# Optimization experiments

Measured on AMD Instinct MI355X. Metric: run time of the kernel, lower is better.

The kernel has to match this reference:

```python
import jax, jax.numpy as jnp
import numpy as np

N = 50000   # nodes
E = 800000  # edges (avg degree 16)
F_IN = 128
D_HID = 128
N_CLASS = 40


def setup_inputs() -> dict:
    key = jax.random.key(0)
    ks = jax.random.split(key, 10)
    s = 0.05
    return {
        "x": jax.random.normal(ks[0], (N, F_IN), jnp.float32),
        "edge_index": jax.random.randint(ks[1], (2, E), 0, N, dtype=jnp.int32),
        "W_in": jax.random.normal(ks[2], (F_IN, D_HID), jnp.float32) * s,
        "b_in": jnp.zeros((D_HID,), jnp.float32),
        "W1": jax.random.normal(ks[3], (D_HID, D_HID), jnp.float32) * s,
        "b1": jnp.zeros((D_HID,), jnp.float32),
        "W2": jax.random.normal(ks[4], (D_HID, D_HID), jnp.float32) * s,
        "b2": jnp.zeros((D_HID,), jnp.float32),
        "W_out": jax.random.normal(ks[5], (D_HID, N_CLASS), jnp.float32) * s,
        "b_out": jnp.zeros((N_CLASS,), jnp.float32),
    }


def _gcn_norm(edge_index, num_nodes):
    # Add self loops, compute symmetric normalization D^-1/2 (A+I) D^-1/2.
    loop = jnp.arange(num_nodes, dtype=edge_index.dtype)
    src = jnp.concatenate([edge_index[0], loop])
    dst = jnp.concatenate([edge_index[1], loop])
    deg = jnp.zeros((num_nodes,), jnp.float32).at[dst].add(1.0)
    dinv = jnp.where(deg > 0, jax.lax.rsqrt(deg), 0.0)
    norm = dinv[src] * dinv[dst]  # [E+N]
    return src, dst, norm


def _gcn_conv(h, W, b, src, dst, norm, num_nodes):
    # transform then sparse aggregate (gather-scale-scatter)
    h = h @ W                                   # [N, d]
    msg = h[src] * norm[:, None]                # [E+N, d]
    agg = jax.ops.segment_sum(msg, dst, num_segments=num_nodes)
    return agg + b


def reference(x, edge_index, W_in, b_in, W1, b1, W2, b2, W_out, b_out):
    num_nodes = x.shape[0]
    src, dst, norm = _gcn_norm(edge_index, num_nodes)
    h = _gcn_conv(x, W_in, b_in, src, dst, norm, num_nodes)
    # eval mode: dropout is identity
    h = jax.nn.relu(_gcn_conv(h, W1, b1, src, dst, norm, num_nodes))
    h = jax.nn.relu(_gcn_conv(h, W2, b2, src, dst, norm, num_nodes))
    out = h @ W_out + b_out
    return jax.nn.log_softmax(out, axis=1)
```

## Files before the change

### kernel.cpp

```cpp
#include <hip/hip_runtime.h>
#include <hip/hip_bf16.h>
#include <math.h>

#define NEG_INF (-3.402823466e38f)
typedef unsigned int uint;
typedef unsigned short ushort;
typedef __attribute__((ext_vector_type(8))) short short8;
typedef __attribute__((ext_vector_type(4))) float f32x4;

__device__ __forceinline__ float bf_lo(uint u) { return __uint_as_float(u << 16); }
__device__ __forceinline__ float bf_hi(uint u) { return __uint_as_float(u & 0xffff0000u); }
__device__ __forceinline__ ushort f2bf(float f) {
  __hip_bfloat16 h = __float2bfloat16(f);
  return *reinterpret_cast<ushort*>(&h);
}
__device__ __forceinline__ uint pack2(float a, float b) {
  return (uint)f2bf(a) | ((uint)f2bf(b) << 16);
}

__global__ __launch_bounds__(256) void k_pcnt(
    const float* __restrict__ W_in, const float* __restrict__ W1,
    const float* __restrict__ W2, ushort* __restrict__ Wt,
    const int* __restrict__ edges, int* __restrict__ cnt8, int E, int n)
{
  int b = blockIdx.x;
  if (b < 24) {
    const float* W = (b < 8) ? W_in : (b < 16) ? W1 : W2;
    ushort* dst = Wt + (size_t)(b >> 3) * 16384;
    int id = (b & 7) * 256 + threadIdx.x;
    int col = id >> 4, kc = id & 15;
    const float* src = W + (size_t)(kc * 8) * 128 + col;
    uint4 pk;
    pk.x = pack2(src[0],       src[128]);
    pk.y = pack2(src[2 * 128], src[3 * 128]);
    pk.z = pack2(src[4 * 128], src[5 * 128]);
    pk.w = pack2(src[6 * 128], src[7 * 128]);
    ((uint4*)dst)[id] = pk;
  } else {
    int cb = b - 24;
    int* my = cnt8 + (size_t)(cb & 7) * n;
    int stride = ((int)gridDim.x - 24) * 256;
    for (int e = cb * 256 + threadIdx.x; e < E; e += stride)
      atomicAdd(&my[edges[E + e]], 1);
  }
}

__global__ void k_dinv(const int* __restrict__ cnt8, int* __restrict__ cnt,
                       float* __restrict__ dinv, int n) {
  int i = blockIdx.x * 256 + threadIdx.x;
  if (i < n) {
    int s = 0;
    #pragma unroll
    for (int p = 0; p < 8; ++p) s += cnt8[(size_t)p * n + i];
    cnt[i] = s;
    dinv[i] = rsqrtf((float)s + 1.0f);
  }
}

__global__ __launch_bounds__(256) void k_gf(
    const float* __restrict__ A, const ushort* __restrict__ Wt,
    const float* __restrict__ dinv, ushort* __restrict__ T, int n, int gb,
    const int* __restrict__ edges, int* __restrict__ cfill,
    int* __restrict__ csr, int E, int npp, int nbp)
{
  __shared__ ushort sW[128 * 128];
  int tid = threadIdx.x;

  if ((int)blockIdx.x >= gb) {
    int b2 = blockIdx.x - gb;
    int part = b2 & 7;
    int lo = part * npp, hi = lo + npp;
    int stride = nbp * 256;
    int e = (b2 >> 3) * 256 + tid;
    for (; e + 3 * stride < E; e += 4 * stride) {
      int d0 = edges[E + e];
      int d1 = edges[E + e + stride];
      int d2 = edges[E + e + 2 * stride];
      int d3 = edges[E + e + 3 * stride];
      if (d0 >= lo && d0 < hi) { int s = edges[e];              int p0 = atomicAdd(&cfill[d0], 1); if (p0 < 64) csr[((size_t)d0 << 6) + p0] = s; }
      if (d1 >= lo && d1 < hi) { int s = edges[e + stride];     int p1 = atomicAdd(&cfill[d1], 1); if (p1 < 64) csr[((size_t)d1 << 6) + p1] = s; }
      if (d2 >= lo && d2 < hi) { int s = edges[e + 2 * stride]; int p2 = atomicAdd(&cfill[d2], 1); if (p2 < 64) csr[((size_t)d2 << 6) + p2] = s; }
      if (d3 >= lo && d3 < hi) { int s = edges[e + 3 * stride]; int p3 = atomicAdd(&cfill[d3], 1); if (p3 < 64) csr[((size_t)d3 << 6) + p3] = s; }
    }
    for (; e < E; e += stride) {
      int d = edges[E + e];
      if (d >= lo && d < hi) { int s = edges[e]; int p0 = atomicAdd(&cfill[d], 1); if (p0 < 64) csr[((size_t)d << 6) + p0] = s; }
    }
    return;
  }

  {
    const uint4* Wt4 = (const uint4*)Wt;
    uint4* sW4 = (uint4*)sW;
    #pragma unroll
    for (int j = 0; j < 8; ++j) {
      int id = j * 256 + tid;
      int col = id >> 4, kc = id & 15;
      sW4[(col << 4) | (kc ^ (col & 7))] = Wt4[id];
    }
  }
  __syncthreads();

  int wid = tid >> 6, lane = tid & 63;
  int lr = lane & 15, lg = lane >> 4;
  int rbase = blockIdx.x * 64 + wid * 16;
  int arow = rbase + lr;
  bool valid = arow < n;

  f32x4 acc[8];
  #pragma unroll
  for (int cf = 0; cf < 8; ++cf) acc[cf] = (f32x4){0.f, 0.f, 0.f, 0.f};

  #pragma unroll
  for (int ks = 0; ks < 4; ++ks) {
    short8 a = {};
    if (valid) {
      const float4* Af = (const float4*)(A + (size_t)arow * 128) + (ks * 4 + lg) * 2;
      float4 u = Af[0], w = Af[1];
      union { uint4 u4; short8 s8; } cv;
      cv.u4.x = pack2(u.x, u.y); cv.u4.y = pack2(u.z, u.w);
      cv.u4.z = pack2(w.x, w.y); cv.u4.w = pack2(w.z, w.w);
      a = cv.s8;
    }
    int kc = (ks << 2) | lg;
    #pragma unroll
    for (int cf = 0; cf < 8; ++cf) {
      int col = (cf << 4) | lr;
      const short8* bp = (const short8*)sW + ((col << 4) | (kc ^ (lr & 7)));
      acc[cf] = __builtin_amdgcn_mfma_f32_16x16x32_bf16(a, *bp, acc[cf], 0, 0, 0);
    }
  }

  #pragma unroll
  for (int v = 0; v < 4; ++v) {
    int row = rbase + (lg << 2) + v;
    if (row < n) {
      float s = dinv[row];
      ushort* dst = T + (size_t)row * 128 + lr;
      #pragma unroll
      for (int cf = 0; cf < 8; ++cf) dst[cf << 4] = f2bf(acc[cf][v] * s);
    }
  }
}

__global__ __launch_bounds__(256) void k_gemm(
    const ushort* __restrict__ Ap, const ushort* __restrict__ Wt,
    const float* __restrict__ dinv, ushort* __restrict__ T, int n)
{
  __shared__ ushort sW[128 * 128];
  int tid = threadIdx.x;
  {
    const uint4* Wt4 = (const uint4*)Wt;
    uint4* sW4 = (uint4*)sW;
    #pragma unroll
    for (int j = 0; j < 8; ++j) {
      int id = j * 256 + tid;
      int col = id >> 4, kc = id & 15;
      sW4[(col << 4) | (kc ^ (col & 7))] = Wt4[id];
    }
  }
  __syncthreads();

  int wid = tid >> 6, lane = tid & 63;
  int lr = lane & 15, lg = lane >> 4;
  int rbase = blockIdx.x * 64 + wid * 16;
  int arow = rbase + lr;
  bool valid = arow < n;

  f32x4 acc[8];
  #pragma unroll
  for (int cf = 0; cf < 8; ++cf) acc[cf] = (f32x4){0.f, 0.f, 0.f, 0.f};

  #pragma unroll
  for (int ks = 0; ks < 4; ++ks) {
    short8 a = {};
    if (valid) a = ((const short8*)(Ap + (size_t)arow * 128))[ks * 4 + lg];
    int kc = (ks << 2) | lg;
    #pragma unroll
    for (int cf = 0; cf < 8; ++cf) {
      int col = (cf << 4) | lr;
      const short8* bp = (const short8*)sW + ((col << 4) | (kc ^ (lr & 7)));
      acc[cf] = __builtin_amdgcn_mfma_f32_16x16x32_bf16(a, *bp, acc[cf], 0, 0, 0);
    }
  }

  #pragma unroll
  for (int v = 0; v < 4; ++v) {
    int row = rbase + (lg << 2) + v;
    if (row < n) {
      float s = dinv[row];
      ushort* dst = T + (size_t)row * 128 + lr;
      #pragma unroll
      for (int cf = 0; cf < 8; ++cf) dst[cf << 4] = f2bf(acc[cf][v] * s);
    }
  }
}

template <int RELU>
__global__ __launch_bounds__(256) void k_agg(
    const ushort* __restrict__ T, const int* __restrict__ cnt,
    const int* __restrict__ csr, const float* __restrict__ dinv,
    const float* __restrict__ bias, ushort* __restrict__ H, int n)
{
  int u = (blockIdx.x << 2) + (threadIdx.x >> 6);
  if (u >= n) return;
  int lane = threadIdx.x & 63;
  const uint* Tu = (const uint*)T;
  uint su = Tu[(size_t)u * 64 + lane];
  float ax = bf_lo(su), ay = bf_hi(su);
  int deg = cnt[u];
  int dcap = deg > 64 ? 64 : deg;
  int eid = (lane < dcap) ? csr[((size_t)u << 6) + lane] : 0;
  int j = 0;
  for (; j + 16 <= dcap; j += 16) {
    uint v[16];
    #pragma unroll
    for (int q = 0; q < 16; ++q) {
      int s = __shfl(eid, j + q);
      v[q] = Tu[(size_t)s * 64 + lane];
    }
    float sx = 0.f, sy = 0.f;
    #pragma unroll
    for (int q = 0; q < 16; ++q) { sx += bf_lo(v[q]); sy += bf_hi(v[q]); }
    ax += sx; ay += sy;
  }
  for (; j + 4 <= dcap; j += 4) {
    int s0 = __shfl(eid, j);     int s1 = __shfl(eid, j + 1);
    int s2 = __shfl(eid, j + 2); int s3 = __shfl(eid, j + 3);
    uint v0 = Tu[(size_t)s0 * 64 + lane];
    uint v1 = Tu[(size_t)s1 * 64 + lane];
    uint v2 = Tu[(size_t)s2 * 64 + lane];
    uint v3 = Tu[(size_t)s3 * 64 + lane];
    ax += (bf_lo(v0) + bf_lo(v1)) + (bf_lo(v2) + bf_lo(v3));
    ay += (bf_hi(v0) + bf_hi(v1)) + (bf_hi(v2) + bf_hi(v3));
  }
  for (; j < dcap; ++j) {
    int s = __shfl(eid, j);
    uint v = Tu[(size_t)s * 64 + lane];
    ax += bf_lo(v); ay += bf_hi(v);
  }
  float du = dinv[u];
  float2 b2 = *(const float2*)(bias + (lane << 1));
  float ox = fmaf(ax, du, b2.x);
  float oy = fmaf(ay, du, b2.y);
  if (RELU) { ox = fmaxf(ox, 0.f); oy = fmaxf(oy, 0.f); }
  ((uint*)H)[(size_t)u * 64 + lane] = pack2(ox, oy);
}

__global__ __launch_bounds__(256) void k_head(
    const ushort* __restrict__ H, const float* __restrict__ Wo,
    const float* __restrict__ bo, float* __restrict__ out, int n)
{
  __shared__ float sWo[128 * 40];
  __shared__ float sX[128 * 64];
  int tid = threadIdx.x;
  int rbase = blockIdx.x * 64;

  {
    const float4* Wo4 = (const float4*)Wo;
    float4* sWo4 = (float4*)sWo;
    #pragma unroll
    for (int i = 0; i < 5; ++i) sWo4[i * 256 + tid] = Wo4[i * 256 + tid];
  }
  {
    const uint4* H4 = (const uint4*)H;
    #pragma unroll
    for (int j = 0; j < 4; ++j) {
      int id = j * 256 + tid;
      int r = id & 63, kc8 = id >> 6;
      int row = rbase + r;
      uint4 v = make_uint4(0u, 0u, 0u, 0u);
      if (row < n) v = H4[(size_t)row * 16 + kc8];
      float f[8] = {bf_lo(v.x), bf_hi(v.x), bf_lo(v.y), bf_hi(v.y),
                    bf_lo(v.z), bf_hi(v.z), bf_lo(v.w), bf_hi(v.w)};
      #pragma unroll
      for (int j2 = 0; j2 < 8; ++j2) {
        int k = kc8 * 8 + j2;
        int swz = ((k >> 2) & 7) << 2;
        sX[k * 64 + (r ^ swz)] = f[j2];
      }
    }
  }
  __syncthreads();

  int cg = tid & 7;
  int rg = tid >> 3;
  float bj[5];
  #pragma unroll
  for (int j = 0; j < 5; ++j) bj[j] = bo[cg * 5 + j];
  float acc[2][5];
  #pragma unroll
  for (int i = 0; i < 2; ++i)
    #pragma unroll
    for (int j = 0; j < 5; ++j) acc[i][j] = bj[j];

  #pragma unroll 4
  for (int k = 0; k < 128; ++k) {
    int swz = ((k >> 2) & 7) << 2;
    float2 xv = *(const float2*)(sX + k * 64 + ((rg << 1) ^ swz));
    const float* wr = sWo + k * 40 + cg * 5;
    float w0 = wr[0], w1 = wr[1], w2 = wr[2], w3 = wr[3], w4 = wr[4];
    acc[0][0] = fmaf(xv.x, w0, acc[0][0]);
    acc[0][1] = fmaf(xv.x, w1, acc[0][1]);
    acc[0][2] = fmaf(xv.x, w2, acc[0][2]);
    acc[0][3] = fmaf(xv.x, w3, acc[0][3]);
    acc[0][4] = fmaf(xv.x, w4, acc[0][4]);
    acc[1][0] = fmaf(xv.y, w0, acc[1][0]);
    acc[1][1] = fmaf(xv.y, w1, acc[1][1]);
    acc[1][2] = fmaf(xv.y, w2, acc[1][2]);
    acc[1][3] = fmaf(xv.y, w3, acc[1][3]);
    acc[1][4] = fmaf(xv.y, w4, acc[1][4]);
  }

  #pragma unroll
  for (int i = 0; i < 2; ++i) {
    int row = rbase + (rg << 1) + i;
    float m = acc[i][0];
    m = fmaxf(m, acc[i][1]); m = fmaxf(m, acc[i][2]);
    m = fmaxf(m, acc[i][3]); m = fmaxf(m, acc[i][4]);
    m = fmaxf(m, __shfl_xor(m, 1));
    m = fmaxf(m, __shfl_xor(m, 2));
    m = fmaxf(m, __shfl_xor(m, 4));
    float s = 0.f;
    #pragma unroll
    for (int j = 0; j < 5; ++j) s += __expf(acc[i][j] - m);
    s += __shfl_xor(s, 1);
    s += __shfl_xor(s, 2);
    s += __shfl_xor(s, 4);
    float ls = m + __logf(s);
    if (row < n) {
      float* dst = out + (size_t)row * 40 + cg * 5;
      #pragma unroll
      for (int j = 0; j < 5; ++j) dst[j] = acc[i][j] - ls;
    }
  }
}

extern "C" void kernel_launch(void* const* d_in, const int* in_sizes, int n_in,
                              void* d_out, int out_size, void* d_ws, size_t ws_size,
                              hipStream_t stream) {
  const float* x    = (const float*)d_in[0];
  const int*   edges= (const int*)d_in[1];
  const float* W_in = (const float*)d_in[2];
  const float* b_in = (const float*)d_in[3];
  const float* W1   = (const float*)d_in[4];
  const float* b1   = (const float*)d_in[5];
  const float* W2   = (const float*)d_in[6];
  const float* b2   = (const float*)d_in[7];
  const float* Wo   = (const float*)d_in[8];
  const float* bo   = (const float*)d_in[9];
  float* out = (float*)d_out;

  int N = in_sizes[0] / 128;
  int E = in_sizes[1] / 2;
  int NB = (N + 255) / 256;

  char* p = (char*)d_ws;
  auto alloc = [&](size_t bytes) {
    char* r = p; p += (bytes + 255) & ~(size_t)255; return r;
  };
  ushort* t    = (ushort*)alloc((size_t)N * 128 * 2);
  ushort* h    = (ushort*)alloc((size_t)N * 128 * 2);
  ushort* wt   = (ushort*)alloc(3 * 16384 * 2);
  int*   cnt8  = (int*)  alloc((size_t)N * 9 * 4);
  int*   cfill = cnt8 + (size_t)N * 8;
  int*   cnt   = (int*)  alloc((size_t)N * 4);
  float* dinv  = (float*)alloc((size_t)N * 4);
  int*   csr   = (int*)  alloc((size_t)N * 64 * 4);
  (void)ws_size; (void)n_in; (void)out_size;

  int NPP = (N + 7) / 8;
  int NBP = 512;
  int GB  = (N + 63) / 64;
  int AB  = (N + 3) / 4;

  hipMemsetAsync(cnt8, 0, (size_t)N * 9 * 4, stream);
  k_pcnt<<<24 + 2048, 256, 0, stream>>>(W_in, W1, W2, wt, edges, cnt8, E, N);
  k_dinv<<<NB, 256, 0, stream>>>(cnt8, cnt, dinv, N);
  k_gf  <<<GB + NBP * 8, 256, 0, stream>>>(x, wt, dinv, t, N, GB,
                                           edges, cfill, csr, E, NPP, NBP);
  k_agg<0><<<AB, 256, 0, stream>>>(t, cnt, csr, dinv, b_in, h, N);
  k_gemm<<<GB, 256, 0, stream>>>(h, wt + 16384, dinv, t, N);
  k_agg<1><<<AB, 256, 0, stream>>>(t, cnt, csr, dinv, b1, h, N);
  k_gemm<<<GB, 256, 0, stream>>>(h, wt + 2 * 16384, dinv, t, N);
  k_agg<1><<<AB, 256, 0, stream>>>(t, cnt, csr, dinv, b2, h, N);
  k_head<<<GB, 256, 0, stream>>>(h, Wo, bo, out, N);
}
```

Baseline: 224.2 us.

## Drop separate degree-count pass; apply source normalization inside aggregation

Removes the separate edge-degree counting kernel and takes degrees from the CSR fill counters, so dinv is computed after the fused GEMM/CSR-build kernel. Because dinv is no longer known when the GEMM runs, source-side scaling moves out of the GEMM epilogues into the aggregation loop. There each neighbor's dinv is gathered once per lane and broadcast by shuffle, and self-loop scaling is handled separately. Weight conversion to bf16 is folded into the fused kernel. This saves one full pass over the edge list of atomics and a memset of eight count copies. In exchange it adds a dinv gather and extra shuffles per edge in every aggregation.

```diff
diff --git a/kernel.cpp b/kernel.cpp
--- a/kernel.cpp
+++ b/kernel.cpp
@@ -18,56 +18,24 @@
   return (uint)f2bf(a) | ((uint)f2bf(b) << 16);
 }
 
-__global__ __launch_bounds__(256) void k_pcnt(
-    const float* __restrict__ W_in, const float* __restrict__ W1,
-    const float* __restrict__ W2, ushort* __restrict__ Wt,
-    const int* __restrict__ edges, int* __restrict__ cnt8, int E, int n)
-{
-  int b = blockIdx.x;
-  if (b < 24) {
-    const float* W = (b < 8) ? W_in : (b < 16) ? W1 : W2;
-    ushort* dst = Wt + (size_t)(b >> 3) * 16384;
-    int id = (b & 7) * 256 + threadIdx.x;
-    int col = id >> 4, kc = id & 15;
-    const float* src = W + (size_t)(kc * 8) * 128 + col;
-    uint4 pk;
-    pk.x = pack2(src[0],       src[128]);
-    pk.y = pack2(src[2 * 128], src[3 * 128]);
-    pk.z = pack2(src[4 * 128], src[5 * 128]);
-    pk.w = pack2(src[6 * 128], src[7 * 128]);
-    ((uint4*)dst)[id] = pk;
-  } else {
-    int cb = b - 24;
-    int* my = cnt8 + (size_t)(cb & 7) * n;
-    int stride = ((int)gridDim.x - 24) * 256;
-    for (int e = cb * 256 + threadIdx.x; e < E; e += stride)
-      atomicAdd(&my[edges[E + e]], 1);
-  }
-}
-
-__global__ void k_dinv(const int* __restrict__ cnt8, int* __restrict__ cnt,
-                       float* __restrict__ dinv, int n) {
+__global__ void k_dinv(const int* __restrict__ cfill, float* __restrict__ dinv, int n) {
   int i = blockIdx.x * 256 + threadIdx.x;
-  if (i < n) {
-    int s = 0;
-    #pragma unroll
-    for (int p = 0; p < 8; ++p) s += cnt8[(size_t)p * n + i];
-    cnt[i] = s;
-    dinv[i] = rsqrtf((float)s + 1.0f);
-  }
+  if (i < n) dinv[i] = rsqrtf((float)cfill[i] + 1.0f);
 }
 
 __global__ __launch_bounds__(256) void k_gf(
-    const float* __restrict__ A, const ushort* __restrict__ Wt,
-    const float* __restrict__ dinv, ushort* __restrict__ T, int n, int gb,
+    const float* __restrict__ A, const float* __restrict__ W_in,
+    const float* __restrict__ W1, const float* __restrict__ W2,
+    ushort* __restrict__ Wt, ushort* __restrict__ T, int n, int gb,
     const int* __restrict__ edges, int* __restrict__ cfill,
     int* __restrict__ csr, int E, int npp, int nbp)
 {
   __shared__ ushort sW[128 * 128];
   int tid = threadIdx.x;
-
-  if ((int)blockIdx.x >= gb) {
-    int b2 = blockIdx.x - gb;
+  int bid = blockIdx.x;
+
+  if (bid >= gb + 16) {
+    int b2 = bid - gb - 16;
     int part = b2 & 7;
     int lo = part * npp, hi = lo + npp;
     int stride = nbp * 256;
@@ -89,21 +57,42 @@
     return;
   }
 
+  if (bid >= gb) {
+    int b2 = bid - gb;
+    const float* W = (b2 < 8) ? W1 : W2;
+    ushort* dst = Wt + (size_t)(b2 >> 3) * 16384;
+    int id = (b2 & 7) * 256 + tid;
+    int col = id >> 4, kc = id & 15;
+    const float* src = W + (size_t)(kc * 8) * 128 + col;
+    uint4 pk;
+    pk.x = pack2(src[0],       src[128]);
+    pk.y = pack2(src[2 * 128], src[3 * 128]);
+    pk.z = pack2(src[4 * 128], src[5 * 128]);
+    pk.w = pack2(src[6 * 128], src[7 * 128]);
+    ((uint4*)dst)[id] = pk;
+    return;
+  }
+
   {
-    const uint4* Wt4 = (const uint4*)Wt;
     uint4* sW4 = (uint4*)sW;
     #pragma unroll
     for (int j = 0; j < 8; ++j) {
       int id = j * 256 + tid;
       int col = id >> 4, kc = id & 15;
-      sW4[(col << 4) | (kc ^ (col & 7))] = Wt4[id];
+      const float* src = W_in + (size_t)(kc * 8) * 128 + col;
+      uint4 pk;
+      pk.x = pack2(src[0],       src[128]);
+      pk.y = pack2(src[2 * 128], src[3 * 128]);
+      pk.z = pack2(src[4 * 128], src[5 * 128]);
+      pk.w = pack2(src[6 * 128], src[7 * 128]);
+      sW4[(col << 4) | (kc ^ (col & 7))] = pk;
     }
   }
   __syncthreads();
 
   int wid = tid >> 6, lane = tid & 63;
   int lr = lane & 15, lg = lane >> 4;
-  int rbase = blockIdx.x * 64 + wid * 16;
+  int rbase = bid * 64 + wid * 16;
   int arow = rbase + lr;
   bool valid = arow < n;
 
@@ -135,17 +124,16 @@
   for (int v = 0; v < 4; ++v) {
     int row = rbase + (lg << 2) + v;
     if (row < n) {
-      float s = dinv[row];
       ushort* dst = T + (size_t)row * 128 + lr;
       #pragma unroll
-      for (int cf = 0; cf < 8; ++cf) dst[cf << 4] = f2bf(acc[cf][v] * s);
+      for (int cf = 0; cf < 8; ++cf) dst[cf << 4] = f2bf(acc[cf][v]);
     }
   }
 }
 
 __global__ __launch_bounds__(256) void k_gemm(
     const ushort* __restrict__ Ap, const ushort* __restrict__ Wt,
-    const float* __restrict__ dinv, ushort* __restrict__ T, int n)
+    ushort* __restrict__ T, int n)
 {
   __shared__ ushort sW[128 * 128];
   int tid = threadIdx.x;
@@ -188,17 +176,16 @@
   for (int v = 0; v < 4; ++v) {
     int row = rbase + (lg << 2) + v;
     if (row < n) {
-      float s = dinv[row];
       ushort* dst = T + (size_t)row * 128 + lr;
       #pragma unroll
-      for (int cf = 0; cf < 8; ++cf) dst[cf << 4] = f2bf(acc[cf][v] * s);
+      for (int cf = 0; cf < 8; ++cf) dst[cf << 4] = f2bf(acc[cf][v]);
     }
   }
 }
 
 template <int RELU>
 __global__ __launch_bounds__(256) void k_agg(
-    const ushort* __restrict__ T, const int* __restrict__ cnt,
+    const ushort* __restrict__ T, const int* __restrict__ cfill,
     const int* __restrict__ csr, const float* __restrict__ dinv,
     const float* __restrict__ bias, ushort* __restrict__ H, int n)
 {
@@ -207,42 +194,53 @@
   int lane = threadIdx.x & 63;
   const uint* Tu = (const uint*)T;
   uint su = Tu[(size_t)u * 64 + lane];
-  float ax = bf_lo(su), ay = bf_hi(su);
-  int deg = cnt[u];
+  int deg = cfill[u];
   int dcap = deg > 64 ? 64 : deg;
-  int eid = (lane < dcap) ? csr[((size_t)u << 6) + lane] : 0;
+  int eid = 0; float ds = 0.f;
+  if (lane < dcap) {
+    eid = csr[((size_t)u << 6) + lane];
+    ds  = dinv[eid];
+  }
+  float ax = 0.f, ay = 0.f;
   int j = 0;
   for (; j + 16 <= dcap; j += 16) {
-    uint v[16];
+    uint v[16]; float w[16];
     #pragma unroll
     for (int q = 0; q < 16; ++q) {
       int s = __shfl(eid, j + q);
+      w[q] = __shfl(ds, j + q);
       v[q] = Tu[(size_t)s * 64 + lane];
     }
-    float sx = 0.f, sy = 0.f;
-    #pragma unroll
-    for (int q = 0; q < 16; ++q) { sx += bf_lo(v[q]); sy += bf_hi(v[q]); }
-    ax += sx; ay += sy;
+    #pragma unroll
+    for (int q = 0; q < 16; ++q) {
+      ax = fmaf(w[q], bf_lo(v[q]), ax);
+      ay = fmaf(w[q], bf_hi(v[q]), ay);
+    }
   }
   for (; j + 4 <= dcap; j += 4) {
-    int s0 = __shfl(eid, j);     int s1 = __shfl(eid, j + 1);
-    int s2 = __shfl(eid, j + 2); int s3 = __shfl(eid, j + 3);
+    int s0 = __shfl(eid, j);     float w0 = __shfl(ds, j);
+    int s1 = __shfl(eid, j + 1); float w1 = __shfl(ds, j + 1);
+    int s2 = __shfl(eid, j + 2); float w2 = __shfl(ds, j + 2);
+    int s3 = __shfl(eid, j + 3); float w3 = __shfl(ds, j + 3);
     uint v0 = Tu[(size_t)s0 * 64 + lane];
     uint v1 = Tu[(size_t)s1 * 64 + lane];
     uint v2 = Tu[(size_t)s2 * 64 + lane];
     uint v3 = Tu[(size_t)s3 * 64 + lane];
-    ax += (bf_lo(v0) + bf_lo(v1)) + (bf_lo(v2) + bf_lo(v3));
-    ay += (bf_hi(v0) + bf_hi(v1)) + (bf_hi(v2) + bf_hi(v3));
+    ax = fmaf(w0, bf_lo(v0), fmaf(w1, bf_lo(v1), fmaf(w2, bf_lo(v2), fmaf(w3, bf_lo(v3), ax))));
+    ay = fmaf(w0, bf_hi(v0), fmaf(w1, bf_hi(v1), fmaf(w2, bf_hi(v2), fmaf(w3, bf_hi(v3), ay))));
   }
   for (; j < dcap; ++j) {
     int s = __shfl(eid, j);
+    float w = __shfl(ds, j);
     uint v = Tu[(size_t)s * 64 + lane];
-    ax += bf_lo(v); ay += bf_hi(v);
+    ax = fmaf(w, bf_lo(v), ax);
+    ay = fmaf(w, bf_hi(v), ay);
   }
   float du = dinv[u];
+  float sw = du * du;
   float2 b2 = *(const float2*)(bias + (lane << 1));
-  float ox = fmaf(ax, du, b2.x);
-  float oy = fmaf(ay, du, b2.y);
+  float ox = fmaf(du, ax, fmaf(sw, bf_lo(su), b2.x));
+  float oy = fmaf(du, ay, fmaf(sw, bf_hi(su), b2.y));
   if (RELU) { ox = fmaxf(ox, 0.f); oy = fmaxf(oy, 0.f); }
   ((uint*)H)[(size_t)u * 64 + lane] = pack2(ox, oy);
 }
@@ -359,14 +357,12 @@
   auto alloc = [&](size_t bytes) {
     char* r = p; p += (bytes + 255) & ~(size_t)255; return r;
   };
-  ushort* t    = (ushort*)alloc((size_t)N * 128 * 2);
-  ushort* h    = (ushort*)alloc((size_t)N * 128 * 2);
-  ushort* wt   = (ushort*)alloc(3 * 16384 * 2);
-  int*   cnt8  = (int*)  alloc((size_t)N * 9 * 4);
-  int*   cfill = cnt8 + (size_t)N * 8;
-  int*   cnt   = (int*)  alloc((size_t)N * 4);
-  float* dinv  = (float*)alloc((size_t)N * 4);
-  int*   csr   = (int*)  alloc((size_t)N * 64 * 4);
+  ushort* t     = (ushort*)alloc((size_t)N * 128 * 2);
+  ushort* h     = (ushort*)alloc((size_t)N * 128 * 2);
+  ushort* wt    = (ushort*)alloc(2 * 16384 * 2);
+  int*    cfill = (int*)  alloc((size_t)N * 4);
+  float*  dinv  = (float*)alloc((size_t)N * 4);
+  int*    csr   = (int*)  alloc((size_t)N * 64 * 4);
   (void)ws_size; (void)n_in; (void)out_size;
 
   int NPP = (N + 7) / 8;
@@ -374,15 +370,14 @@
   int GB  = (N + 63) / 64;
   int AB  = (N + 3) / 4;
 
-  hipMemsetAsync(cnt8, 0, (size_t)N * 9 * 4, stream);
-  k_pcnt<<<24 + 2048, 256, 0, stream>>>(W_in, W1, W2, wt, edges, cnt8, E, N);
-  k_dinv<<<NB, 256, 0, stream>>>(cnt8, cnt, dinv, N);
-  k_gf  <<<GB + NBP * 8, 256, 0, stream>>>(x, wt, dinv, t, N, GB,
-                                           edges, cfill, csr, E, NPP, NBP);
-  k_agg<0><<<AB, 256, 0, stream>>>(t, cnt, csr, dinv, b_in, h, N);
-  k_gemm<<<GB, 256, 0, stream>>>(h, wt + 16384, dinv, t, N);
-  k_agg<1><<<AB, 256, 0, stream>>>(t, cnt, csr, dinv, b1, h, N);
-  k_gemm<<<GB, 256, 0, stream>>>(h, wt + 2 * 16384, dinv, t, N);
-  k_agg<1><<<AB, 256, 0, stream>>>(t, cnt, csr, dinv, b2, h, N);
+  hipMemsetAsync(cfill, 0, (size_t)N * 4, stream);
+  k_gf  <<<GB + 16 + NBP * 8, 256, 0, stream>>>(x, W_in, W1, W2, wt, t, N, GB,
+                                                edges, cfill, csr, E, NPP, NBP);
+  k_dinv<<<NB, 256, 0, stream>>>(cfill, dinv, N);
+  k_agg<0><<<AB, 256, 0, stream>>>(t, cfill, csr, dinv, b_in, h, N);
+  k_gemm<<<GB, 256, 0, stream>>>(h, wt, t, N);
+  k_agg<1><<<AB, 256, 0, stream>>>(t, cfill, csr, dinv, b1, h, N);
+  k_gemm<<<GB, 256, 0, stream>>>(h, wt + 16384, t, N);
+  k_agg<1><<<AB, 256, 0, stream>>>(t, cfill, csr, dinv, b2, h, N);
   k_head<<<GB, 256, 0, stream>>>(h, Wo, bo, out, N);
 }
```

After: 224.0 us. No clear change (-0.1%).
